# Optimization experiments

Measured on AMD Instinct MI355X. Metric: run time of the kernel, lower is better.

The kernel has to match this reference:

```python
import jax, jax.numpy as jnp
import numpy as np

N = 100000   # n_nodes (= ninput, identity features)
E = 1600000  # edges per adjacency (avg degree 16)
H = 128      # nhid
EPS = 1e-12


def setup_inputs() -> dict:
    key = jax.random.key(0)
    ks = jax.random.split(key, 24)
    inp = {
        'adj1_rows': jax.random.randint(ks[0], (E,), 0, N),
        'adj1_cols': jax.random.randint(ks[1], (E,), 0, N),
        'adj1_vals': jax.random.uniform(ks[2], (E,), jnp.float32) / 16.0,
        'adj2_rows': jax.random.randint(ks[3], (E,), 0, N),
        'adj2_cols': jax.random.randint(ks[4], (E,), 0, N),
        'adj2_vals': jax.random.uniform(ks[5], (E,), jnp.float32) / 16.0,
    }
    s = 1.0 / np.sqrt(H)
    inp['w1'] = jax.random.uniform(ks[6], (N, H), jnp.float32, -s, s)
    for i in range(2, 10):
        inp[f'w{i}'] = jax.random.uniform(ks[5 + i], (H, H), jnp.float32, -s, s)
    s2 = 1.0 / np.sqrt(2 * H)
    inp['m1'] = jax.random.uniform(ks[15], (H, 2 * H), jnp.float32, -s, s)
    inp['b1'] = jnp.zeros((2 * H,), jnp.float32)
    inp['m2'] = jax.random.uniform(ks[16], (2 * H, 2 * H), jnp.float32, -s2, s2)
    inp['b2'] = jnp.zeros((2 * H,), jnp.float32)
    inp['m3'] = jax.random.uniform(ks[17], (2 * H, 1), jnp.float32, -s2, s2)
    inp['b3'] = jnp.zeros((1,), jnp.float32)
    return inp


def _spmm(rows, cols, vals, x):
    # sparse [N,N] @ dense [N,H] via gather + segment_sum
    return jax.ops.segment_sum(vals[:, None] * x[cols], rows, num_segments=N)


def _l2norm(x):
    # F.normalize(x, p=2, dim=1)
    n = jnp.sqrt(jnp.sum(x * x, axis=1, keepdims=True))
    return x / jnp.maximum(n, EPS)


def _mlp(x, m1, b1, m2, b2, m3, b3):
    # dropout inactive (eval mode) for deterministic reference
    h = jax.nn.relu(x @ m1 + b1)
    h = jax.nn.relu(h @ m2 + b2)
    return h @ m3 + b3  # [N,1]


def _branch(rows, cols, vals, w1, ws, mlp_params):
    x = jax.nn.relu(_spmm(rows, cols, vals, w1))
    x = _l2norm(x)
    score = _mlp(x, *mlp_params)
    for i, w in enumerate(ws):
        x = jax.nn.relu(_spmm(rows, cols, vals, x @ w))
        if i < len(ws) - 1:  # last layer (gc9) is relu only, no normalize
            x = _l2norm(x)
        score = score + _mlp(x, *mlp_params)
    return score


def reference(adj1_rows, adj1_cols, adj1_vals, adj2_rows, adj2_cols, adj2_vals,
              w1, w2, w3, w4, w5, w6, w7, w8, w9,
              m1, b1, m2, b2, m3, b3):
    ws = [w2, w3, w4, w5, w6, w7, w8, w9]
    mlp_params = (m1, b1, m2, b2, m3, b3)
    score1 = _branch(adj1_rows, adj1_cols, adj1_vals, w1, ws, mlp_params)
    score2 = _branch(adj2_rows, adj2_cols, adj2_vals, w1, ws, mlp_params)
    return score1 * score2  # [N,1]
```

## Files before the change

### kernel.cpp

```cpp
#include <hip/hip_runtime.h>
#include <hip/hip_fp16.h>

#define NN 100000
#define NE 1600000
#define HD 128
#define HD2 256

#define NBK 512
#define RPB 196
#define CH  4096
#define CAP 4096

typedef unsigned int u32;
typedef unsigned short u16;
typedef _Float16 half8 __attribute__((ext_vector_type(8)));
typedef float floatx4 __attribute__((ext_vector_type(4)));

static inline int cdiv(int a, int b){ return (a + b - 1) / b; }

__device__ __forceinline__ u32 split_pack(float v){
  __half h;
  if(fabsf(v) < 6.103515625e-05f) h = __ushort_as_half((u16)0);
  else h = __float2half_rn(v);
  float hf = __half2float(h);
  __half l = __float2half_rn((v - hf) * 4096.0f);
  return (u32)__half_as_ushort(h) | ((u32)__half_as_ushort(l) << 16);
}

__global__ void k_setup(const float* __restrict__ w0, const float* __restrict__ w1,
                        const float* __restrict__ w2, const float* __restrict__ w3,
                        const float* __restrict__ w4, const float* __restrict__ w5,
                        const float* __restrict__ w6, const float* __restrict__ w7,
                        const float* __restrict__ m1, const float* __restrict__ m2,
                        u32* __restrict__ wbase, float* __restrict__ sc,
                        int* __restrict__ bcur){
  int bid = blockIdx.x;
  if(bid < 896){
    int idx = bid * 256 + threadIdx.x;
    const float* W; int K, N, local;
    if(idx < 131072){
      int wi = idx >> 14; local = idx & 16383; K = HD; N = HD;
      W = wi == 0 ? w0 : wi == 1 ? w1 : wi == 2 ? w2 : wi == 3 ? w3 :
          wi == 4 ? w4 : wi == 5 ? w5 : wi == 6 ? w6 : w7;
    } else if(idx < 163840){
      local = idx - 131072; K = HD; N = HD2; W = m1;
    } else {
      local = idx - 163840; K = HD2; N = HD2; W = m2;
    }
    int n = local / K, k = local - n * K;
    wbase[idx] = split_pack(W[(size_t)k * N + n]);
  } else if(bid < 896 + 782){
    int i = (bid - 896) * 256 + threadIdx.x;
    if(i < 2 * NN) sc[i] = 0.f;
  } else {
    int i = (bid - 896 - 782) * 256 + threadIdx.x;
    if(i < 2 * NBK) bcur[i] = (i & (NBK - 1)) * CAP;
  }
}

__global__ void k_binscatter(const int* __restrict__ r0a, const int* __restrict__ c0a,
                             const float* __restrict__ v0a,
                             const int* __restrict__ r1a, const int* __restrict__ c1a,
                             const float* __restrict__ v1a,
                             int* __restrict__ bcur,
                             u32* __restrict__ sr0, uint2* __restrict__ sv0,
                             u32* __restrict__ sr1, uint2* __restrict__ sv1){
  __shared__ int cnt[NBK];
  __shared__ int bstart[NBK];
  __shared__ int gbase[NBK];
  __shared__ int sh[256];
  __shared__ u32 srow[CH];
  __shared__ uint2 scvs[CH];
  int z = blockIdx.y;
  const int* rows = z ? r1a : r0a;
  const int* cols = z ? c1a : c0a;
  const float* vals = z ? v1a : v0a;
  int* cur = bcur + z * NBK;
  u32* osr = z ? sr1 : sr0;
  uint2* osv = z ? sv1 : sv0;
  int t = threadIdx.x;
  for(int i = t; i < NBK; i += 256) cnt[i] = 0;
  __syncthreads();
  int e0 = blockIdx.x * CH;
  int total = NE - e0; if(total > CH) total = CH;
  int r_[16], c_[16], b_[16], k_[16]; float v_[16];
  #pragma unroll
  for(int k = 0; k < 16; k++){
    int e = e0 + t + k * 256;
    b_[k] = -1;
    if(e < NE){
      r_[k] = rows[e]; c_[k] = cols[e]; v_[k] = vals[e];
      b_[k] = r_[k] / RPB;
      k_[k] = atomicAdd(&cnt[b_[k]], 1);
    }
  }
  __syncthreads();
  int v0 = cnt[2 * t], v1 = cnt[2 * t + 1];
  int s2 = v0 + v1;
  sh[t] = s2;
  __syncthreads();
  for(int d = 1; d < 256; d <<= 1){
    int tv = (t >= d) ? sh[t - d] : 0;
    __syncthreads();
    sh[t] += tv;
    __syncthreads();
  }
  int excl = sh[t] - s2;
  bstart[2 * t] = excl;
  bstart[2 * t + 1] = excl + v0;
  __syncthreads();
  #pragma unroll
  for(int k = 0; k < 16; k++){
    if(b_[k] >= 0){
      int slot = bstart[b_[k]] + k_[k];
      srow[slot] = (u32)r_[k];
      scvs[slot] = make_uint2((u32)c_[k], __float_as_uint(v_[k]));
    }
  }
  for(int b = t; b < NBK; b += 256){
    int c = cnt[b];
    if(c > 0) gbase[b] = atomicAdd(&cur[b], c);
  }
  __syncthreads();
  for(int i = t; i < total; i += 256){
    u32 r = srow[i];
    int b = (int)r / RPB;
    int dest = gbase[b] + (i - bstart[b]);
    osr[dest] = r;
    osv[dest] = scvs[i];
  }
}

__global__ void k_bucket_scan(const int* __restrict__ bcur, int* __restrict__ bbase,
                              int* __restrict__ c1ptr, int* __restrict__ c2ptr){
  __shared__ int sh[256];
  int z = blockIdx.x;
  const int* cur = bcur + z * NBK;
  int* bb = bbase + z * NBK;
  int t = threadIdx.x;
  int v0 = cur[2 * t]     - (2 * t) * CAP;
  int v1 = cur[2 * t + 1] - (2 * t + 1) * CAP;
  int s2 = v0 + v1;
  sh[t] = s2;
  __syncthreads();
  for(int d = 1; d < 256; d <<= 1){
    int tv = (t >= d) ? sh[t - d] : 0;
    __syncthreads();
    sh[t] += tv;
    __syncthreads();
  }
  int excl = sh[t] - s2;
  bb[2 * t] = excl;
  bb[2 * t + 1] = excl + v0;
  if(t == 0){
    int* rp = z ? c2ptr : c1ptr;
    rp[NN] = NE;
  }
}

__global__ void k_bucket_place(const int* __restrict__ bcur, const int* __restrict__ bbase,
                               const u32* __restrict__ sr0, const uint2* __restrict__ sv0,
                               const u32* __restrict__ sr1, const uint2* __restrict__ sv1,
                               int* __restrict__ c1ptr, int* __restrict__ c2ptr,
                               uint2* __restrict__ e0, uint2* __restrict__ e1){
  __shared__ int hist[RPB];
  __shared__ int cur[RPB];
  __shared__ int sh[256];
  __shared__ u32 srows[CAP];
  int z = blockIdx.y;
  int b = blockIdx.x;
  int r0 = b * RPB;
  if(r0 >= NN) return;
  int rend = r0 + RPB; if(rend > NN) rend = NN;
  int nr = rend - r0;
  const u32* sr = z ? sr1 : sr0;
  const uint2* sv = z ? sv1 : sv0;
  int* rp = z ? c2ptr : c1ptr;
  uint2* ecv = z ? e1 : e0;
  int cnt = bcur[z * NBK + b] - b * CAP;
  int base = bbase[z * NBK + b];
  int g = b * CAP;
  int t = threadIdx.x;
  for(int r = t; r < nr; r += 256) hist[r] = 0;
  __syncthreads();
  for(int i = t; i < cnt; i += 256){
    u32 r = sr[g + i];
    srows[i] = r;
    atomicAdd(&hist[(int)r - r0], 1);
  }
  __syncthreads();
  int v = (t < nr) ? hist[t] : 0;
  sh[t] = v;
  __syncthreads();
  for(int d = 1; d < 256; d <<= 1){
    int tv = (t >= d) ? sh[t - d] : 0;
    __syncthreads();
    sh[t] += tv;
    __syncthreads();
  }
  int excl = sh[t] - v;
  if(t < nr){
    rp[r0 + t] = base + excl;
    cur[t] = base + excl;
  }
  __syncthreads();
  for(int i = t; i < cnt; i += 256){
    int r = (int)srows[i] - r0;
    int p = atomicAdd(&cur[r], 1);
    ecv[p] = sv[g + i];
  }
}

template<bool NORM>
__global__ void k_spmm(const int* __restrict__ rowptr, const uint2* __restrict__ ecv,
                       const float* __restrict__ X, u32* __restrict__ outpk){
  int node = (blockIdx.x << 2) + (threadIdx.x >> 6);
  int lane = threadIdx.x & 63;
  if(node >= NN) return;
  int s = rowptr[node], e = rowptr[node + 1];
  float ax = 0.f, ay = 0.f, bx = 0.f, by = 0.f;
  int i = s;
  for(; i + 15 < e; i += 16){
    uint2 ee[16]; float2 xx[16];
    #pragma unroll
    for(int j = 0; j < 16; j++) ee[j] = ecv[i + j];
    #pragma unroll
    for(int j = 0; j < 16; j++) xx[j] = *(const float2*)(X + (size_t)ee[j].x * HD + lane * 2);
    #pragma unroll
    for(int j = 0; j < 16; j += 4){
      ax += __uint_as_float(ee[j].y)   * xx[j].x   + __uint_as_float(ee[j+1].y) * xx[j+1].x;
      ay += __uint_as_float(ee[j].y)   * xx[j].y   + __uint_as_float(ee[j+1].y) * xx[j+1].y;
      bx += __uint_as_float(ee[j+2].y) * xx[j+2].x + __uint_as_float(ee[j+3].y) * xx[j+3].x;
      by += __uint_as_float(ee[j+2].y) * xx[j+2].y + __uint_as_float(ee[j+3].y) * xx[j+3].y;
    }
  }
  for(; i + 3 < e; i += 4){
    uint2 f0 = ecv[i], f1 = ecv[i+1], f2 = ecv[i+2], f3 = ecv[i+3];
    float2 x0 = *(const float2*)(X + (size_t)f0.x * HD + lane * 2);
    float2 x1 = *(const float2*)(X + (size_t)f1.x * HD + lane * 2);
    float2 x2 = *(const float2*)(X + (size_t)f2.x * HD + lane * 2);
    float2 x3 = *(const float2*)(X + (size_t)f3.x * HD + lane * 2);
    ax += __uint_as_float(f0.y) * x0.x + __uint_as_float(f1.y) * x1.x;
    ay += __uint_as_float(f0.y) * x0.y + __uint_as_float(f1.y) * x1.y;
    bx += __uint_as_float(f2.y) * x2.x + __uint_as_float(f3.y) * x3.x;
    by += __uint_as_float(f2.y) * x2.y + __uint_as_float(f3.y) * x3.y;
  }
  for(; i < e; i++){
    uint2 f0 = ecv[i];
    float2 xv = *(const float2*)(X + (size_t)f0.x * HD + lane * 2);
    ax += __uint_as_float(f0.y) * xv.x;
    ay += __uint_as_float(f0.y) * xv.y;
  }
  ax += bx; ay += by;
  ax = fmaxf(ax, 0.f);
  ay = fmaxf(ay, 0.f);
  if(NORM){
    float ss = ax * ax + ay * ay;
    #pragma unroll
    for(int o = 32; o >= 1; o >>= 1) ss += __shfl_xor(ss, o, 64);
    float scale = 1.f / fmaxf(sqrtf(ss), 1e-12f);
    ax *= scale; ay *= scale;
  }
  *(uint2*)(outpk + (size_t)node * HD + lane * 2) = make_uint2(split_pack(ax), split_pack(ay));
}

template<int MODE>
__launch_bounds__(256, 2)
__global__ void k_mfma_gemm(const u32* __restrict__ Apk, const u32* __restrict__ Btpk,
                            const u32* __restrict__ Bt1pk,
                            const float* __restrict__ bias, float* __restrict__ Yout,
                            u32* __restrict__ Hout, const float* __restrict__ m3,
                            float* __restrict__ score, int M, int K, int N){
  __shared__ u16 As_h[128 * 40], As_l[128 * 40];
  __shared__ u16 Bs_h[128 * 40], Bs_l[128 * 40];
  constexpr int NYC = (MODE == 0) ? 1 : ((MODE == 3) ? 3 : 2);
  const int d = blockIdx.x;
  const int grp = d / (8 * NYC);
  const int rem = d - grp * 8 * NYC;
  const int rt = grp * 8 + (rem & 7);
  const int ct = rem >> 3;
  const int nrt = (M + 127) >> 7;
  if(rt >= nrt) return;
  const int tid = threadIdx.x;
  const int lane = tid & 63, wid = tid >> 6;
  const int lm = lane & 15, lg = lane >> 4;
  const int mq = (wid & 1) * 64, nq = (wid >> 1) * 64;
  const int m0 = rt * 128;
  int n0 = ct * 128;
  const u32* Bt = Btpk;
  bool m0path = true;
  if(MODE == 3){
    m0path = (ct == 0);
    if(m0path){ n0 = 0; }
    else      { n0 = (ct - 1) * 128; Bt = Bt1pk; }
  }

  floatx4 accA[4][4], accB[4][4];
  #pragma unroll
  for(int i = 0; i < 4; i++)
    #pragma unroll
    for(int j = 0; j < 4; j++){
      accA[i][j] = (floatx4){0.f, 0.f, 0.f, 0.f};
      accB[i][j] = (floatx4){0.f, 0.f, 0.f, 0.f};
    }

  for(int k0 = 0; k0 < K; k0 += 32){
    uint4 av[4], bv[4];
    #pragma unroll
    for(int j = 0; j < 4; j++){
      int li = tid + j * 256;
      int row = li >> 3, kc = (li & 7) * 4;
      int ar = m0 + row; if(ar >= M) ar = M - 1;
      av[j] = *(const uint4*)(Apk + (size_t)ar * K + k0 + kc);
      bv[j] = *(const uint4*)(Bt + (size_t)(n0 + row) * K + k0 + kc);
    }
    if(k0) __syncthreads();
    #pragma unroll
    for(int j = 0; j < 4; j++){
      int li = tid + j * 256;
      int row = li >> 3, kc = (li & 7) * 4;
      int base = row * 40 + kc;
      ushort4 h, l;
      h.x = (u16)(av[j].x & 0xffff); l.x = (u16)(av[j].x >> 16);
      h.y = (u16)(av[j].y & 0xffff); l.y = (u16)(av[j].y >> 16);
      h.z = (u16)(av[j].z & 0xffff); l.z = (u16)(av[j].z >> 16);
      h.w = (u16)(av[j].w & 0xffff); l.w = (u16)(av[j].w >> 16);
      *(ushort4*)&As_h[base] = h;
      *(ushort4*)&As_l[base] = l;
      h.x = (u16)(bv[j].x & 0xffff); l.x = (u16)(bv[j].x >> 16);
      h.y = (u16)(bv[j].y & 0xffff); l.y = (u16)(bv[j].y >> 16);
      h.z = (u16)(bv[j].z & 0xffff); l.z = (u16)(bv[j].z >> 16);
      h.w = (u16)(bv[j].w & 0xffff); l.w = (u16)(bv[j].w >> 16);
      *(ushort4*)&Bs_h[base] = h;
      *(ushort4*)&Bs_l[base] = l;
    }
    __syncthreads();

    half8 fa_h[4], fa_l[4], fb_h[4], fb_l[4];
    #pragma unroll
    for(int s = 0; s < 4; s++){
      int ra = (mq + s * 16 + lm) * 40 + lg * 8;
      fa_h[s] = *(const half8*)&As_h[ra];
      fa_l[s] = *(const half8*)&As_l[ra];
      int rb = (nq + s * 16 + lm) * 40 + lg * 8;
      fb_h[s] = *(const half8*)&Bs_h[rb];
      fb_l[s] = *(const half8*)&Bs_l[rb];
    }
    #pragma unroll
    for(int i = 0; i < 4; i++)
      #pragma unroll
      for(int j = 0; j < 4; j++){
        accA[i][j] = __builtin_amdgcn_mfma_f32_16x16x32_f16(fa_h[i], fb_h[j], accA[i][j], 0, 0, 0);
        accB[i][j] = __builtin_amdgcn_mfma_f32_16x16x32_f16(fa_h[i], fb_l[j], accB[i][j], 0, 0, 0);
        accB[i][j] = __builtin_amdgcn_mfma_f32_16x16x32_f16(fa_l[i], fb_h[j], accB[i][j], 0, 0, 0);
      }
  }

  const float inv4096 = 1.f / 4096.f;
  if(MODE == 0 || (MODE == 3 && m0path)){
    int ldy = (MODE == 3) ? HD : N;
    #pragma unroll
    for(int i = 0; i < 4; i++)
      #pragma unroll
      for(int r = 0; r < 4; r++){
        int m = m0 + mq + i * 16 + lg * 4 + r;
        if(m < M){
          #pragma unroll
          for(int j = 0; j < 4; j++){
            int c = n0 + nq + j * 16 + lm;
            Yout[(size_t)m * ldy + c] = accA[i][j][r] + accB[i][j][r] * inv4096;
          }
        }
      }
  } else if(MODE == 1 || MODE == 3){
    int ldh = (MODE == 3) ? HD2 : N;
    #pragma unroll
    for(int i = 0; i < 4; i++)
      #pragma unroll
      for(int r = 0; r < 4; r++){
        int m = m0 + mq + i * 16 + lg * 4 + r;
        if(m < M){
          #pragma unroll
          for(int j = 0; j < 4; j++){
            int c = n0 + nq + j * 16 + lm;
            float v = fmaxf(accA[i][j][r] + accB[i][j][r] * inv4096 + bias[c], 0.f);
            Hout[(size_t)m * ldh + c] = split_pack(v);
          }
        }
      }
  } else {
    #pragma unroll
    for(int i = 0; i < 4; i++)
      #pragma unroll
      for(int r = 0; r < 4; r++){
        float s = 0.f;
        #pragma unroll
        for(int j = 0; j < 4; j++){
          int c = n0 + nq + j * 16 + lm;
          float v = fmaxf(accA[i][j][r] + accB[i][j][r] * inv4096 + bias[c], 0.f);
          s = fmaf(v, m3[c], s);
        }
        s += __shfl_xor(s, 1, 64);
        s += __shfl_xor(s, 2, 64);
        s += __shfl_xor(s, 4, 64);
        s += __shfl_xor(s, 8, 64);
        int m = m0 + mq + i * 16 + lg * 4 + r;
        if(lm == 0 && m < M) atomicAdd(&score[m], s);
      }
  }
}

__global__ void k_final(const float* __restrict__ sc, const float* __restrict__ b3,
                        float* __restrict__ out){
  int i = blockIdx.x * 256 + threadIdx.x;
  if(i < NN){
    float b = 9.f * b3[0];
    out[i] = (sc[i] + b) * (sc[NN + i] + b);
  }
}

extern "C" void kernel_launch(void* const* d_in, const int* in_sizes, int n_in,
                              void* d_out, int out_size, void* d_ws, size_t ws_size,
                              hipStream_t stream){
  const int*   a1r = (const int*)d_in[0];
  const int*   a1c = (const int*)d_in[1];
  const float* a1v = (const float*)d_in[2];
  const int*   a2r = (const int*)d_in[3];
  const int*   a2c = (const int*)d_in[4];
  const float* a2v = (const float*)d_in[5];
  const float* w1  = (const float*)d_in[6];
  const float* w[8];
  for(int i = 0; i < 8; i++) w[i] = (const float*)d_in[7 + i];
  const float* m1 = (const float*)d_in[15];
  const float* b1 = (const float*)d_in[16];
  const float* m2 = (const float*)d_in[17];
  const float* b2 = (const float*)d_in[18];
  const float* m3 = (const float*)d_in[19];
  const float* b3 = (const float*)d_in[20];
  float* out = (float*)d_out;

  char* base = (char*)d_ws;
  size_t off = 0;
  auto alloc = [&](size_t bytes) -> char* {
    char* r = base + off;
    off += (bytes + 255) & ~(size_t)255;
    return r;
  };
  int*   c1ptr = (int*)  alloc((size_t)(NN + 1) * 4);
  int*   c2ptr = (int*)  alloc((size_t)(NN + 1) * 4);
  uint2* ecv1  = (uint2*)alloc((size_t)NE * 8);
  uint2* ecv2  = (uint2*)alloc((size_t)NE * 8);
  int*   cursor= (int*)  alloc((size_t)2 * NBK * 4);
  int*   bbase = (int*)  alloc((size_t)2 * NBK * 4);
  float* sc    = (float*)alloc((size_t)2 * NN * 4);
  u32*   wtpk[8];
  for(int i = 0; i < 8; i++) wtpk[i] = (u32*)alloc((size_t)HD * HD * 4);
  u32*   m1tpk = (u32*)alloc((size_t)HD2 * HD * 4);
  u32*   m2tpk = (u32*)alloc((size_t)HD2 * HD2 * 4);
  u32*   xpk   = (u32*)alloc((size_t)NN * HD * 4);
  u32*   h1pk  = (u32*)alloc((size_t)NN * HD2 * 4);
  size_t need_ded = off + (((size_t)NN * HD * 4 + 255) & ~(size_t)255);
  bool ded_y = (ws_size >= need_ded);
  float* y = ded_y ? (float*)alloc((size_t)NN * HD * 4) : (float*)h1pk;

  const size_t SZ = (size_t)NBK * CAP;
  char* hb = (char*)h1pk;
  uint2* sv1 = (uint2*)hb;
  u32*   sr1 = (u32*)(hb + SZ * 8);
  uint2* sv2 = (uint2*)(hb + SZ * 12);
  u32*   sr2 = (u32*)(hb + SZ * 20);

  hipLaunchKernelGGL(k_setup, dim3(896 + 782 + 4), dim3(256), 0, stream,
                     w[0], w[1], w[2], w[3], w[4], w[5], w[6], w[7], m1, m2,
                     wtpk[0], sc, cursor);
  hipLaunchKernelGGL(k_binscatter, dim3(cdiv(NE, CH), 2), dim3(256), 0, stream,
                     a1r, a1c, a1v, a2r, a2c, a2v, cursor, sr1, sv1, sr2, sv2);
  hipLaunchKernelGGL(k_bucket_scan, dim3(2), dim3(256), 0, stream, cursor, bbase, c1ptr, c2ptr);
  hipLaunchKernelGGL(k_bucket_place, dim3(NBK, 2), dim3(256), 0, stream,
                     cursor, bbase, sr1, sv1, sr2, sv2, c1ptr, c2ptr, ecv1, ecv2);

  const int NRT = cdiv(NN, 128);
  const int GP  = cdiv(NRT, 8) * 8;
  const int SPB = cdiv(NN, 4);
  auto mode1 = [&](){
    hipLaunchKernelGGL((k_mfma_gemm<1>), dim3(GP * 2), dim3(256), 0, stream,
                       xpk, m1tpk, (const u32*)nullptr, b1, (float*)nullptr, h1pk,
                       (const float*)nullptr, (float*)nullptr, NN, HD, HD2);
  };
  auto mode2 = [&](float* score){
    hipLaunchKernelGGL((k_mfma_gemm<2>), dim3(GP * 2), dim3(256), 0, stream,
                       h1pk, m2tpk, (const u32*)nullptr, b2, (float*)nullptr, (u32*)nullptr,
                       m3, score, NN, HD2, HD2);
  };
  auto gemm0 = [&](int i){
    hipLaunchKernelGGL((k_mfma_gemm<0>), dim3(GP * 1), dim3(256), 0, stream,
                       xpk, wtpk[i], (const u32*)nullptr, (const float*)nullptr, y, (u32*)nullptr,
                       (const float*)nullptr, (float*)nullptr, NN, HD, HD);
  };
  auto fused01 = [&](int i){
    hipLaunchKernelGGL((k_mfma_gemm<3>), dim3(GP * 3), dim3(256), 0, stream,
                       xpk, wtpk[i], m1tpk, b1, y, h1pk,
                       (const float*)nullptr, (float*)nullptr, NN, HD, 0);
  };

  for(int b = 0; b < 2; b++){
    const int* rp = b ? c2ptr : c1ptr;
    const uint2* ecv = b ? ecv2 : ecv1;
    float* score = sc + (size_t)b * NN;
    hipLaunchKernelGGL((k_spmm<true>), dim3(SPB), dim3(256), 0, stream,
                       rp, ecv, w1, xpk);
    if(ded_y){
      for(int i = 0; i < 8; i++){
        fused01(i);
        mode2(score);
        if(i < 7)
          hipLaunchKernelGGL((k_spmm<true>),  dim3(SPB), dim3(256), 0, stream,
                             rp, ecv, y, xpk);
        else
          hipLaunchKernelGGL((k_spmm<false>), dim3(SPB), dim3(256), 0, stream,
                             rp, ecv, y, xpk);
      }
      mode1();
      mode2(score);
    } else {
      mode1();
      mode2(score);
      for(int i = 0; i < 8; i++){
        gemm0(i);
        if(i < 7)
          hipLaunchKernelGGL((k_spmm<true>),  dim3(SPB), dim3(256), 0, stream,
                             rp, ecv, y, xpk);
        else
          hipLaunchKernelGGL((k_spmm<false>), dim3(SPB), dim3(256), 0, stream,
                             rp, ecv, y, xpk);
        mode1();
        mode2(score);
      }
    }
  }

  hipLaunchKernelGGL(k_final, dim3(cdiv(NN, 256)), dim3(256), 0, stream, sc, b3, out);
}
```

Before: 4.266 ms.

## Sort edges by column per row in LDS and split SpMM wave into half-waves

The bucket placement kernel now stages edges in shared memory, insertion-sorts each row's edges by column index, then writes them out contiguously. The write is coalesced and the gathers become more ordered for locality. The SpMM kernel now has each half-wave handle alternate edges with float4 loads per lane, then combines the halves with a cross-half shuffle. This doubles the independent gathers in flight. The costs are more LDS use in the placement kernel, which can lower occupancy, plus serial insertion-sort work and a changed summation order.

```diff
diff --git a/kernel.cpp b/kernel.cpp
--- a/kernel.cpp
+++ b/kernel.cpp
@@ -165,8 +165,10 @@
                                uint2* __restrict__ e0, uint2* __restrict__ e1){
   __shared__ int hist[RPB];
   __shared__ int cur[RPB];
+  __shared__ int rs[RPB + 1];
   __shared__ int sh[256];
   __shared__ u32 srows[CAP];
+  __shared__ uint2 est[CAP];
   int z = blockIdx.y;
   int b = blockIdx.x;
   int r0 = b * RPB;
@@ -201,14 +203,28 @@
   int excl = sh[t] - v;
   if(t < nr){
     rp[r0 + t] = base + excl;
-    cur[t] = base + excl;
-  }
+    cur[t] = excl;
+    rs[t] = excl;
+  }
+  if(t == 0) rs[nr] = cnt;
   __syncthreads();
   for(int i = t; i < cnt; i += 256){
     int r = (int)srows[i] - r0;
     int p = atomicAdd(&cur[r], 1);
-    ecv[p] = sv[g + i];
-  }
+    est[p] = sv[g + i];
+  }
+  __syncthreads();
+  for(int r = t; r < nr; r += 256){
+    int lo = rs[r], hi = lo + hist[r];
+    for(int a = lo + 1; a < hi; a++){
+      uint2 key = est[a];
+      int bb2 = a - 1;
+      while(bb2 >= lo && est[bb2].x > key.x){ est[bb2 + 1] = est[bb2]; bb2--; }
+      est[bb2 + 1] = key;
+    }
+  }
+  __syncthreads();
+  for(int i = t; i < cnt; i += 256) ecv[base + i] = est[i];
 }
 
 template<bool NORM>
@@ -217,51 +233,55 @@
   int node = (blockIdx.x << 2) + (threadIdx.x >> 6);
   int lane = threadIdx.x & 63;
   if(node >= NN) return;
-  int s = rowptr[node], e = rowptr[node + 1];
-  float ax = 0.f, ay = 0.f, bx = 0.f, by = 0.f;
-  int i = s;
-  for(; i + 15 < e; i += 16){
-    uint2 ee[16]; float2 xx[16];
-    #pragma unroll
-    for(int j = 0; j < 16; j++) ee[j] = ecv[i + j];
-    #pragma unroll
-    for(int j = 0; j < 16; j++) xx[j] = *(const float2*)(X + (size_t)ee[j].x * HD + lane * 2);
-    #pragma unroll
-    for(int j = 0; j < 16; j += 4){
-      ax += __uint_as_float(ee[j].y)   * xx[j].x   + __uint_as_float(ee[j+1].y) * xx[j+1].x;
-      ay += __uint_as_float(ee[j].y)   * xx[j].y   + __uint_as_float(ee[j+1].y) * xx[j+1].y;
-      bx += __uint_as_float(ee[j+2].y) * xx[j+2].x + __uint_as_float(ee[j+3].y) * xx[j+3].x;
-      by += __uint_as_float(ee[j+2].y) * xx[j+2].y + __uint_as_float(ee[j+3].y) * xx[j+3].y;
-    }
-  }
-  for(; i + 3 < e; i += 4){
-    uint2 f0 = ecv[i], f1 = ecv[i+1], f2 = ecv[i+2], f3 = ecv[i+3];
-    float2 x0 = *(const float2*)(X + (size_t)f0.x * HD + lane * 2);
-    float2 x1 = *(const float2*)(X + (size_t)f1.x * HD + lane * 2);
-    float2 x2 = *(const float2*)(X + (size_t)f2.x * HD + lane * 2);
-    float2 x3 = *(const float2*)(X + (size_t)f3.x * HD + lane * 2);
-    ax += __uint_as_float(f0.y) * x0.x + __uint_as_float(f1.y) * x1.x;
-    ay += __uint_as_float(f0.y) * x0.y + __uint_as_float(f1.y) * x1.y;
-    bx += __uint_as_float(f2.y) * x2.x + __uint_as_float(f3.y) * x3.x;
-    by += __uint_as_float(f2.y) * x2.y + __uint_as_float(f3.y) * x3.y;
-  }
-  for(; i < e; i++){
-    uint2 f0 = ecv[i];
-    float2 xv = *(const float2*)(X + (size_t)f0.x * HD + lane * 2);
-    ax += __uint_as_float(f0.y) * xv.x;
-    ay += __uint_as_float(f0.y) * xv.y;
-  }
-  ax += bx; ay += by;
-  ax = fmaxf(ax, 0.f);
-  ay = fmaxf(ay, 0.f);
+  int h = lane >> 5, s = lane & 31;
+  int sb = rowptr[node], e = rowptr[node + 1];
+  float ax = 0.f, ay = 0.f, az = 0.f, aw = 0.f;
+  int i = sb;
+  for(; i + 7 < e; i += 8){
+    uint2 ee[4]; float4 xx[4];
+    #pragma unroll
+    for(int j = 0; j < 4; j++) ee[j] = ecv[i + 2 * j + h];
+    #pragma unroll
+    for(int j = 0; j < 4; j++) xx[j] = *(const float4*)(X + (size_t)ee[j].x * HD + s * 4);
+    #pragma unroll
+    for(int j = 0; j < 4; j++){
+      float vv = __uint_as_float(ee[j].y);
+      ax = fmaf(vv, xx[j].x, ax);
+      ay = fmaf(vv, xx[j].y, ay);
+      az = fmaf(vv, xx[j].z, az);
+      aw = fmaf(vv, xx[j].w, aw);
+    }
+  }
+  for(; i < e; i += 2){
+    int idx = i + h;
+    bool ok = idx < e;
+    uint2 f = ecv[ok ? idx : i];
+    float vv = ok ? __uint_as_float(f.y) : 0.f;
+    float4 xv = *(const float4*)(X + (size_t)f.x * HD + s * 4);
+    ax = fmaf(vv, xv.x, ax);
+    ay = fmaf(vv, xv.y, ay);
+    az = fmaf(vv, xv.z, az);
+    aw = fmaf(vv, xv.w, aw);
+  }
+  ax += __shfl_xor(ax, 32, 64);
+  ay += __shfl_xor(ay, 32, 64);
+  az += __shfl_xor(az, 32, 64);
+  aw += __shfl_xor(aw, 32, 64);
+  ax = fmaxf(ax, 0.f); ay = fmaxf(ay, 0.f);
+  az = fmaxf(az, 0.f); aw = fmaxf(aw, 0.f);
   if(NORM){
-    float ss = ax * ax + ay * ay;
-    #pragma unroll
-    for(int o = 32; o >= 1; o >>= 1) ss += __shfl_xor(ss, o, 64);
+    float ss = ax * ax + ay * ay + az * az + aw * aw;
+    #pragma unroll
+    for(int o = 16; o >= 1; o >>= 1) ss += __shfl_xor(ss, o, 64);
     float scale = 1.f / fmaxf(sqrtf(ss), 1e-12f);
-    ax *= scale; ay *= scale;
-  }
-  *(uint2*)(outpk + (size_t)node * HD + lane * 2) = make_uint2(split_pack(ax), split_pack(ay));
+    ax *= scale; ay *= scale; az *= scale; aw *= scale;
+  }
+  if(h == 0){
+    uint4 p;
+    p.x = split_pack(ax); p.y = split_pack(ay);
+    p.z = split_pack(az); p.w = split_pack(aw);
+    *(uint4*)(outpk + (size_t)node * HD + s * 4) = p;
+  }
 }
 
 template<int MODE>
```

New measurement: 4.268 ms. About the same (+0.0%).
